# Optimization experiments

Hardware: AMD Instinct MI355X
Metric: run time of the kernel (lower is better)

Reference implementation:

```python
import jax, jax.numpy as jnp
import numpy as np

VOCAB = 256
PAD = 0
D_MODEL = 512
ATTN_DIM = 64
B, L = 8, 2048
LN_EPS = 1e-5


def layer_norm(x, g, b):
    mu = jnp.mean(x, axis=-1, keepdims=True)
    var = jnp.mean(jnp.square(x - mu), axis=-1, keepdims=True)
    return (x - mu) * jax.lax.rsqrt(var + LN_EPS) * g + b


def setup_inputs() -> dict:
    key = jax.random.key(0)
    ks = jax.random.split(key, 10)
    tokens = jax.random.randint(ks[0], (B, L), 1, VOCAB)  # avoid PAD=0
    prefix_lens = jax.random.randint(ks[1], (B,), 256, 1536)
    embed_w = jax.random.normal(ks[2], (VOCAB, D_MODEL), jnp.float32) * 0.02
    embed_w = embed_w.at[PAD].set(0.0)  # padding_idx row
    en_g = jnp.ones((D_MODEL,), jnp.float32)
    en_b = jnp.zeros((D_MODEL,), jnp.float32)
    fn_g = jnp.ones((D_MODEL,), jnp.float32)
    fn_b = jnp.zeros((D_MODEL,), jnp.float32)
    q_w = jax.random.normal(ks[3], (ATTN_DIM, D_MODEL), jnp.float32) * 0.02
    q_b = jnp.zeros((ATTN_DIM,), jnp.float32)
    k_w = jax.random.normal(ks[4], (ATTN_DIM, D_MODEL), jnp.float32) * 0.02
    k_b = jnp.zeros((ATTN_DIM,), jnp.float32)
    g_w = jax.random.normal(ks[5], (1, D_MODEL), jnp.float32) * 0.02
    g_b = jnp.full((1,), 2.0, jnp.float32)  # gate bias init to 2.0
    return dict(tokens=tokens, prefix_lens=prefix_lens, embed_w=embed_w,
                en_g=en_g, en_b=en_b, fn_g=fn_g, fn_b=fn_b,
                q_w=q_w, q_b=q_b, k_w=k_w, k_b=k_b, g_w=g_w, g_b=g_b)


def reference(tokens, prefix_lens, embed_w, en_g, en_b, fn_g, fn_b,
              q_w, q_b, k_w, k_b, g_w, g_b):
    # encode (n_layers=0: embed -> embed_norm -> final_norm)
    x = embed_w[tokens]                       # (B, L, D)
    x = layer_norm(x, en_g, en_b)
    h = layer_norm(x, fn_g, fn_b)

    vocab_logits = jnp.einsum('bld,vd->blv', h, embed_w)   # tied head
    q = h @ q_w.T + q_b                       # (B, L, A)
    k = h @ k_w.T + k_b                       # (B, L, A)
    scores = jnp.einsum('btd,bsd->bts', q, k) / np.sqrt(ATTN_DIM).astype(np.float32)

    idx = jnp.arange(L)[None, :]              # (1, L)
    prefix_mask = (idx < prefix_lens[:, None]) & (tokens != PAD)  # (B, L)
    scores = jnp.where(prefix_mask[:, None, :], scores, -jnp.inf)
    attn = jax.nn.softmax(scores, axis=-1)    # (B, L, L)

    prefix_onehot = jax.nn.one_hot(tokens, VOCAB, dtype=jnp.float32)
    prefix_onehot = prefix_onehot * prefix_mask[..., None]
    copy_dist = jnp.einsum('bts,bsv->btv', attn, prefix_onehot)  # (B, L, V)

    gate = jax.nn.sigmoid(h @ g_w.T + g_b)    # (B, L, 1)
    vocab_probs = jax.nn.softmax(vocab_logits, axis=-1)
    mixed = gate * vocab_probs + (1.0 - gate) * copy_dist
    mixed = jnp.clip(mixed, 1e-12, None)
    return jnp.log(mixed), gate[..., 0], attn
```

## Files before the change

### kernel.cpp

```cpp
#include <hip/hip_runtime.h>
#include <math.h>


#define DM 512
#define VC 256
#define SL 2048
#define NB 8
#define AD 64

typedef float f4v __attribute__((ext_vector_type(4)));

__device__ __forceinline__ float wave_sum(float v) {
#pragma unroll
  for (int o = 32; o > 0; o >>= 1) v += __shfl_xor(v, o, 64);
  return v;
}
__device__ __forceinline__ float wave_max(float v) {
#pragma unroll
  for (int o = 32; o > 0; o >>= 1) v = fmaxf(v, __shfl_xor(v, o, 64));
  return v;
}
__device__ __forceinline__ float blk_sum(float v, float* red) {
  v = wave_sum(v);
  if ((threadIdx.x & 63) == 0) red[threadIdx.x >> 6] = v;
  __syncthreads();
  float r = red[0] + red[1] + red[2] + red[3];
  __syncthreads();
  return r;
}
__device__ __forceinline__ float blk_max(float v, float* red) {
  v = wave_max(v);
  if ((threadIdx.x & 63) == 0) red[threadIdx.x >> 6] = v;
  __syncthreads();
  float r = fmaxf(fmaxf(red[0], red[1]), fmaxf(red[2], red[3]));
  __syncthreads();
  return r;
}

__global__ __launch_bounds__(256) void kprep(
    const float* __restrict__ embed_w, const float* __restrict__ q_w,
    const float* __restrict__ k_w, const int* __restrict__ tokens,
    const int* __restrict__ prefix_lens,
    float* __restrict__ embed_P, float* __restrict__ qk_P,
    int* __restrict__ cnt, int* __restrict__ ncnt,
    int* __restrict__ offs, int* __restrict__ list)
{
  __shared__ int c[VC];
  __shared__ int ca[VC];
  __shared__ int off[VC];
  __shared__ int cur[VC];
  const int blk = blockIdx.x;
  const int tid = threadIdx.x;
  if (blk < DM) {
    const int d = blk;
    embed_P[(((d >> 2) * VC + tid) << 2) + (d & 3)] = embed_w[tid * DM + d];
    if (tid < 128) {
      float val = (tid < 64) ? q_w[tid * DM + d] : k_w[(tid - 64) * DM + d];
      qk_P[(((d >> 2) * 128 + tid) << 2) + (d & 3)] = val;
    }
  } else {
    const int b = blk - DM;
    c[tid] = 0; ca[tid] = 0;
    __syncthreads();
    const int P = prefix_lens[b];
    const int4* trow = (const int4*)(tokens + b * SL);
#pragma unroll
    for (int i = tid; i < SL / 4; i += 256) {
      int4 tk = trow[i];
      int s0 = i * 4;
      atomicAdd(&ca[tk.x], 1); atomicAdd(&ca[tk.y], 1);
      atomicAdd(&ca[tk.z], 1); atomicAdd(&ca[tk.w], 1);
      if (s0     < P && tk.x != 0) atomicAdd(&c[tk.x], 1);
      if (s0 + 1 < P && tk.y != 0) atomicAdd(&c[tk.y], 1);
      if (s0 + 2 < P && tk.z != 0) atomicAdd(&c[tk.z], 1);
      if (s0 + 3 < P && tk.w != 0) atomicAdd(&c[tk.w], 1);
    }
    __syncthreads();
    int myc = ca[tid];
    off[tid] = myc;
    __syncthreads();
    for (int d2 = 1; d2 < VC; d2 <<= 1) {
      int add = (tid >= d2) ? off[tid - d2] : 0;
      __syncthreads();
      off[tid] += add;
      __syncthreads();
    }
    int excl = off[tid] - myc;
    cur[tid] = excl;
    __syncthreads();
#pragma unroll
    for (int i = tid; i < SL / 4; i += 256) {
      int4 tk = trow[i];
      int s0 = i * 4;
      int p;
      p = atomicAdd(&cur[tk.x], 1); list[b * SL + p] = s0;
      p = atomicAdd(&cur[tk.y], 1); list[b * SL + p] = s0 + 1;
      p = atomicAdd(&cur[tk.z], 1); list[b * SL + p] = s0 + 2;
      p = atomicAdd(&cur[tk.w], 1); list[b * SL + p] = s0 + 3;
    }
    __syncthreads();
    cnt [b * VC + tid] = c[tid];
    ncnt[b * VC + tid] = myc;
    offs[b * VC + tid] = excl;
  }
}

__global__ __launch_bounds__(256) void ktok(
    const float* __restrict__ embed_w,
    const float* __restrict__ en_g, const float* __restrict__ en_b,
    const float* __restrict__ fn_g, const float* __restrict__ fn_b,
    const float* __restrict__ q_b, const float* __restrict__ k_b,
    const float* __restrict__ g_w, const float* __restrict__ g_b,
    const float* __restrict__ embed_P, const float* __restrict__ qk_P,
    float* __restrict__ q_tok, float* __restrict__ kT_P,
    float* __restrict__ gate_tok, float* __restrict__ probs_tok)
{
  __shared__ float red[4];
  __shared__ __align__(16) float hs[DM];
  const int tt = blockIdx.x;
  const int tid = threadIdx.x;

  float x0 = embed_w[tt * DM + tid];
  float x1 = embed_w[tt * DM + 256 + tid];
  float mu = blk_sum(x0 + x1, red) * (1.0f / DM);
  float d0 = x0 - mu, d1 = x1 - mu;
  float var = blk_sum(d0 * d0 + d1 * d1, red) * (1.0f / DM);
  float inv = 1.0f / sqrtf(var + 1e-5f);
  float y0 = d0 * inv * en_g[tid] + en_b[tid];
  float y1 = d1 * inv * en_g[tid + 256] + en_b[tid + 256];
  mu = blk_sum(y0 + y1, red) * (1.0f / DM);
  d0 = y0 - mu; d1 = y1 - mu;
  var = blk_sum(d0 * d0 + d1 * d1, red) * (1.0f / DM);
  inv = 1.0f / sqrtf(var + 1e-5f);
  float h0 = d0 * inv * fn_g[tid] + fn_b[tid];
  float h1 = d1 * inv * fn_g[tid + 256] + fn_b[tid + 256];
  hs[tid] = h0; hs[tid + 256] = h1;
  float gp = blk_sum(h0 * g_w[tid] + h1 * g_w[tid + 256], red);
  if (tid == 0) gate_tok[tt] = 1.0f / (1.0f + expf(-(gp + g_b[0])));

  const float4* hs4 = (const float4*)hs;
  const float4* w4p = (const float4*)qk_P;
  const float4* e4p = (const float4*)embed_P;
  const bool qk_lane = (tid < 128);
  float acc = 0.0f;
  float lt = 0.0f;
#pragma unroll 8
  for (int d4 = 0; d4 < DM / 4; ++d4) {
    float4 h4 = hs4[d4];
    float4 e4 = e4p[d4 * VC + tid];
    lt += h4.x * e4.x + h4.y * e4.y + h4.z * e4.z + h4.w * e4.w;
    if (qk_lane) {
      float4 w4 = w4p[d4 * 128 + tid];
      acc += h4.x * w4.x + h4.y * w4.y + h4.z * w4.z + h4.w * w4.w;
    }
  }
  if (qk_lane) {
    if (tid < 64) {
      q_tok[tt * AD + tid] = acc + q_b[tid];
    } else {
      int a = tid - 64;
      kT_P[(((a >> 2) * VC + tt) << 2) + (a & 3)] = acc + k_b[a];
    }
  }
  float m = blk_max(lt, red);
  float e = expf(lt - m);
  float Z = blk_sum(e, red);
  probs_tok[tt * VC + tid] = e / Z;
}

__global__ __launch_bounds__(256) void kfused(
    const float* __restrict__ q_tok, const float* __restrict__ kT_P,
    const int* __restrict__ cnt, const int* __restrict__ ncnt,
    const int* __restrict__ offs, const int* __restrict__ list,
    const float* __restrict__ gate_tok, const float* __restrict__ probs_tok,
    const int* __restrict__ tokens, const int* __restrict__ prefix_lens,
    float* __restrict__ out_logmix, float* __restrict__ out_gate,
    float* __restrict__ out_attn)
{
  __shared__ float red[4];
  __shared__ __align__(16) float qs[AD];
  __shared__ __align__(16) float erow[VC];
  const int b = blockIdx.x >> 8, tt = blockIdx.x & 255;
  const int tid = threadIdx.x;

  const int P = prefix_lens[b];
  const int4* tokrow = (const int4*)(tokens + b * SL);
  int4 tk0 = tokrow[tid];
  int4 tk1 = tokrow[tid + 256];
  const int nr = ncnt[b * VC + tt];
  const int base_off = offs[b * VC + tt];
  const float pv = probs_tok[tt * VC + tid];
  const float g = gate_tok[tt];
  if (tid < AD) qs[tid] = q_tok[tt * AD + tid];
  __syncthreads();

  const float4* qs4 = (const float4*)qs;
  const float4* k4p = (const float4*)kT_P;
  float sv = 0.0f;
#pragma unroll
  for (int a4 = 0; a4 < AD / 4; ++a4) {
    float4 q4 = qs4[a4];
    float4 k4 = k4p[a4 * VC + tid];
    sv += q4.x * k4.x + q4.y * k4.y + q4.z * k4.z + q4.w * k4.w;
  }
  sv *= 0.125f;
  int c = cnt[b * VC + tid];
  float m = blk_max(c > 0 ? sv : -1e30f, red);
  float e = expf(sv - m);
  float Z = blk_sum((float)c * e, red);
  float en = e / Z;
  erow[tid] = en;
  float lv = logf(fmaxf(g * pv + (1.0f - g) * ((float)c * en), 1e-12f));
  __syncthreads();

  f4v a0, a1;
  {
    int s0 = tid * 4;
    a0.x = (s0     < P && tk0.x != 0) ? erow[tk0.x] : 0.0f;
    a0.y = (s0 + 1 < P && tk0.y != 0) ? erow[tk0.y] : 0.0f;
    a0.z = (s0 + 2 < P && tk0.z != 0) ? erow[tk0.z] : 0.0f;
    a0.w = (s0 + 3 < P && tk0.w != 0) ? erow[tk0.w] : 0.0f;
  }
  {
    int s0 = (tid + 256) * 4;
    a1.x = (s0     < P && tk1.x != 0) ? erow[tk1.x] : 0.0f;
    a1.y = (s0 + 1 < P && tk1.y != 0) ? erow[tk1.y] : 0.0f;
    a1.z = (s0 + 2 < P && tk1.z != 0) ? erow[tk1.z] : 0.0f;
    a1.w = (s0 + 3 < P && tk1.w != 0) ? erow[tk1.w] : 0.0f;
  }

  const int* lp = list + b * SL + base_off;
  for (int r = 0; r < nr; ++r) {
    int t = lp[r];
    size_t row = (size_t)(b * SL + t);
    __builtin_nontemporal_store(lv, &out_logmix[row * VC + tid]);
    if (tid == 0) out_gate[row] = g;
    f4v* ar = (f4v*)(out_attn + row * SL);
    __builtin_nontemporal_store(a0, &ar[tid]);
    __builtin_nontemporal_store(a1, &ar[tid + 256]);
  }
}

extern "C" void kernel_launch(void* const* d_in, const int* in_sizes, int n_in,
                              void* d_out, int out_size, void* d_ws, size_t ws_size,
                              hipStream_t stream)
{
  const int*   tokens      = (const int*)  d_in[0];
  const int*   prefix_lens = (const int*)  d_in[1];
  const float* embed_w     = (const float*)d_in[2];
  const float* en_g        = (const float*)d_in[3];
  const float* en_b        = (const float*)d_in[4];
  const float* fn_g        = (const float*)d_in[5];
  const float* fn_b        = (const float*)d_in[6];
  const float* q_b         = (const float*)d_in[8];
  const float* k_b         = (const float*)d_in[10];
  const float* q_w         = (const float*)d_in[7];
  const float* k_w         = (const float*)d_in[9];
  const float* g_w         = (const float*)d_in[11];
  const float* g_b         = (const float*)d_in[12];

  float* ws        = (float*)d_ws;
  float* embed_P   = ws;
  float* qk_P      = embed_P + DM * VC;
  float* kT_P      = qk_P + DM * 128;
  float* q_tok     = kT_P + AD * VC;
  float* gate_tok  = q_tok + VC * AD;
  float* probs_tok = gate_tok + VC;
  int*   cnt       = (int*)(probs_tok + VC * VC);
  int*   ncnt      = cnt + NB * VC;
  int*   offs      = ncnt + NB * VC;
  int*   list      = offs + NB * VC;

  float* out_logmix = (float*)d_out;
  float* out_gate   = out_logmix + (size_t)NB * SL * VC;
  float* out_attn   = out_gate + (size_t)NB * SL;

  kprep<<<DM + NB, 256, 0, stream>>>(embed_w, q_w, k_w, tokens, prefix_lens,
                                     embed_P, qk_P, cnt, ncnt, offs, list);
  ktok<<<VC, 256, 0, stream>>>(embed_w, en_g, en_b, fn_g, fn_b, q_b, k_b,
                               g_w, g_b, embed_P, qk_P,
                               q_tok, kT_P, gate_tok, probs_tok);
  kfused<<<NB * VC, 256, 0, stream>>>(q_tok, kT_P, cnt, ncnt, offs, list,
                                      gate_tok, probs_tok, tokens, prefix_lens,
                                      out_logmix, out_gate, out_attn);
}
```

Before: 238.5 us.

## Process four tokens per block in ktok and use single-wave blocks in kfused

ktok now handles four vocab tokens per 256-thread block, one wave each for the layer norms, and shares every embed_P/qk_P load across the four tokens. This cuts weight traffic and replaces block reductions with wave shuffles. kfused moves to 64-thread blocks where one wave computes all 256 scores and scatters wider rows, so its block-level syncs disappear. The trade is fewer resident threads per block and more registers per thread, while the output-write loop stays memory-bound.

```diff
diff --git a/kernel.cpp b/kernel.cpp
--- a/kernel.cpp
+++ b/kernel.cpp
@@ -20,20 +20,22 @@
   for (int o = 32; o > 0; o >>= 1) v = fmaxf(v, __shfl_xor(v, o, 64));
   return v;
 }
-__device__ __forceinline__ float blk_sum(float v, float* red) {
-  v = wave_sum(v);
-  if ((threadIdx.x & 63) == 0) red[threadIdx.x >> 6] = v;
-  __syncthreads();
-  float r = red[0] + red[1] + red[2] + red[3];
-  __syncthreads();
+__device__ __forceinline__ float hsum4(float4 a) {
+  return a.x + a.y + a.z + a.w;
+}
+__device__ __forceinline__ float4 subs4(float4 a, float s) {
+  float4 r; r.x = a.x - s; r.y = a.y - s; r.z = a.z - s; r.w = a.w - s;
   return r;
 }
-__device__ __forceinline__ float blk_max(float v, float* red) {
-  v = wave_max(v);
-  if ((threadIdx.x & 63) == 0) red[threadIdx.x >> 6] = v;
-  __syncthreads();
-  float r = fmaxf(fmaxf(red[0], red[1]), fmaxf(red[2], red[3]));
-  __syncthreads();
+__device__ __forceinline__ float dot44(float4 a, float4 b) {
+  return a.x * b.x + a.y * b.y + a.z * b.z + a.w * b.w;
+}
+__device__ __forceinline__ float4 lnmap4(float4 d, float inv, float4 g, float4 b) {
+  float4 r;
+  r.x = d.x * inv * g.x + b.x;
+  r.y = d.y * inv * g.y + b.y;
+  r.z = d.z * inv * g.z + b.z;
+  r.w = d.w * inv * g.w + b.w;
   return r;
 }
 
@@ -115,60 +117,90 @@
     float* __restrict__ q_tok, float* __restrict__ kT_P,
     float* __restrict__ gate_tok, float* __restrict__ probs_tok)
 {
-  __shared__ float red[4];
-  __shared__ __align__(16) float hs[DM];
-  const int tt = blockIdx.x;
+  __shared__ __align__(16) float hs[4 * DM];
+  __shared__ __align__(16) float lts[4 * VC];
+  const int t0 = blockIdx.x * 4;
   const int tid = threadIdx.x;
-
-  float x0 = embed_w[tt * DM + tid];
-  float x1 = embed_w[tt * DM + 256 + tid];
-  float mu = blk_sum(x0 + x1, red) * (1.0f / DM);
-  float d0 = x0 - mu, d1 = x1 - mu;
-  float var = blk_sum(d0 * d0 + d1 * d1, red) * (1.0f / DM);
+  const int w = tid >> 6;
+  const int l = tid & 63;
+  const int tt = t0 + w;
+
+  const float4* ew4 = (const float4*)(embed_w + (size_t)tt * DM);
+  float4 x0 = ew4[l];
+  float4 x1 = ew4[l + 64];
+  float mu = wave_sum(hsum4(x0) + hsum4(x1)) * (1.0f / DM);
+  float4 d0 = subs4(x0, mu), d1 = subs4(x1, mu);
+  float var = wave_sum(dot44(d0, d0) + dot44(d1, d1)) * (1.0f / DM);
   float inv = 1.0f / sqrtf(var + 1e-5f);
-  float y0 = d0 * inv * en_g[tid] + en_b[tid];
-  float y1 = d1 * inv * en_g[tid + 256] + en_b[tid + 256];
-  mu = blk_sum(y0 + y1, red) * (1.0f / DM);
-  d0 = y0 - mu; d1 = y1 - mu;
-  var = blk_sum(d0 * d0 + d1 * d1, red) * (1.0f / DM);
+  float4 y0 = lnmap4(d0, inv, ((const float4*)en_g)[l],      ((const float4*)en_b)[l]);
+  float4 y1 = lnmap4(d1, inv, ((const float4*)en_g)[l + 64], ((const float4*)en_b)[l + 64]);
+  mu = wave_sum(hsum4(y0) + hsum4(y1)) * (1.0f / DM);
+  d0 = subs4(y0, mu); d1 = subs4(y1, mu);
+  var = wave_sum(dot44(d0, d0) + dot44(d1, d1)) * (1.0f / DM);
   inv = 1.0f / sqrtf(var + 1e-5f);
-  float h0 = d0 * inv * fn_g[tid] + fn_b[tid];
-  float h1 = d1 * inv * fn_g[tid + 256] + fn_b[tid + 256];
-  hs[tid] = h0; hs[tid + 256] = h1;
-  float gp = blk_sum(h0 * g_w[tid] + h1 * g_w[tid + 256], red);
-  if (tid == 0) gate_tok[tt] = 1.0f / (1.0f + expf(-(gp + g_b[0])));
+  float4 h0 = lnmap4(d0, inv, ((const float4*)fn_g)[l],      ((const float4*)fn_b)[l]);
+  float4 h1 = lnmap4(d1, inv, ((const float4*)fn_g)[l + 64], ((const float4*)fn_b)[l + 64]);
+  float gp = wave_sum(dot44(h0, ((const float4*)g_w)[l]) +
+                      dot44(h1, ((const float4*)g_w)[l + 64]));
+  if (l == 0) gate_tok[tt] = 1.0f / (1.0f + expf(-(gp + g_b[0])));
+  ((float4*)hs)[w * 128 + l]      = h0;
+  ((float4*)hs)[w * 128 + 64 + l] = h1;
+  __syncthreads();
 
   const float4* hs4 = (const float4*)hs;
+  const float4* e4p = (const float4*)embed_P;
   const float4* w4p = (const float4*)qk_P;
-  const float4* e4p = (const float4*)embed_P;
   const bool qk_lane = (tid < 128);
-  float acc = 0.0f;
-  float lt = 0.0f;
-#pragma unroll 8
+  float lt[4] = {0.f, 0.f, 0.f, 0.f};
+  float aq[4] = {0.f, 0.f, 0.f, 0.f};
+#pragma unroll 4
   for (int d4 = 0; d4 < DM / 4; ++d4) {
-    float4 h4 = hs4[d4];
     float4 e4 = e4p[d4 * VC + tid];
-    lt += h4.x * e4.x + h4.y * e4.y + h4.z * e4.z + h4.w * e4.w;
+    float4 hA = hs4[d4];
+    float4 hB = hs4[128 + d4];
+    float4 hC = hs4[256 + d4];
+    float4 hD = hs4[384 + d4];
+    lt[0] += dot44(hA, e4);
+    lt[1] += dot44(hB, e4);
+    lt[2] += dot44(hC, e4);
+    lt[3] += dot44(hD, e4);
     if (qk_lane) {
       float4 w4 = w4p[d4 * 128 + tid];
-      acc += h4.x * w4.x + h4.y * w4.y + h4.z * w4.z + h4.w * w4.w;
-    }
-  }
-  if (qk_lane) {
-    if (tid < 64) {
-      q_tok[tt * AD + tid] = acc + q_b[tid];
-    } else {
-      int a = tid - 64;
-      kT_P[(((a >> 2) * VC + tt) << 2) + (a & 3)] = acc + k_b[a];
-    }
-  }
-  float m = blk_max(lt, red);
-  float e = expf(lt - m);
-  float Z = blk_sum(e, red);
-  probs_tok[tt * VC + tid] = e / Z;
-}
-
-__global__ __launch_bounds__(256) void kfused(
+      aq[0] += dot44(hA, w4);
+      aq[1] += dot44(hB, w4);
+      aq[2] += dot44(hC, w4);
+      aq[3] += dot44(hD, w4);
+    }
+  }
+  if (tid < 64) {
+    float qb = q_b[tid];
+#pragma unroll
+    for (int t = 0; t < 4; ++t) q_tok[(t0 + t) * AD + tid] = aq[t] + qb;
+  } else if (tid < 128) {
+    int a = tid - 64;
+    float kb = k_b[a];
+#pragma unroll
+    for (int t = 0; t < 4; ++t)
+      kT_P[(((a >> 2) * VC + (t0 + t)) << 2) + (a & 3)] = aq[t] + kb;
+  }
+#pragma unroll
+  for (int t = 0; t < 4; ++t) lts[t * VC + tid] = lt[t];
+  __syncthreads();
+
+  float p0 = lts[w * VC + l];
+  float p1 = lts[w * VC + 64 + l];
+  float p2 = lts[w * VC + 128 + l];
+  float p3 = lts[w * VC + 192 + l];
+  float m = wave_max(fmaxf(fmaxf(p0, p1), fmaxf(p2, p3)));
+  float e0 = expf(p0 - m), e1 = expf(p1 - m), e2 = expf(p2 - m), e3 = expf(p3 - m);
+  float Z = wave_sum(e0 + e1 + e2 + e3);
+  probs_tok[tt * VC + l]       = e0 / Z;
+  probs_tok[tt * VC + 64 + l]  = e1 / Z;
+  probs_tok[tt * VC + 128 + l] = e2 / Z;
+  probs_tok[tt * VC + 192 + l] = e3 / Z;
+}
+
+__global__ __launch_bounds__(64) void kfused(
     const float* __restrict__ q_tok, const float* __restrict__ kT_P,
     const int* __restrict__ cnt, const int* __restrict__ ncnt,
     const int* __restrict__ offs, const int* __restrict__ list,
@@ -177,67 +209,85 @@
     float* __restrict__ out_logmix, float* __restrict__ out_gate,
     float* __restrict__ out_attn)
 {
-  __shared__ float red[4];
   __shared__ __align__(16) float qs[AD];
   __shared__ __align__(16) float erow[VC];
+  __shared__ __align__(16) float lvs[VC];
   const int b = blockIdx.x >> 8, tt = blockIdx.x & 255;
-  const int tid = threadIdx.x;
+  const int l = threadIdx.x;
 
   const int P = prefix_lens[b];
   const int4* tokrow = (const int4*)(tokens + b * SL);
-  int4 tk0 = tokrow[tid];
-  int4 tk1 = tokrow[tid + 256];
+  int4 tk[8];
+#pragma unroll
+  for (int i = 0; i < 8; ++i) tk[i] = tokrow[l + (i << 6)];
   const int nr = ncnt[b * VC + tt];
   const int base_off = offs[b * VC + tt];
-  const float pv = probs_tok[tt * VC + tid];
   const float g = gate_tok[tt];
-  if (tid < AD) qs[tid] = q_tok[tt * AD + tid];
+  int   c_[4];
+  float pv[4];
+#pragma unroll
+  for (int j = 0; j < 4; ++j) {
+    c_[j] = cnt[b * VC + l + (j << 6)];
+    pv[j] = probs_tok[tt * VC + l + (j << 6)];
+  }
+  qs[l] = q_tok[tt * AD + l];
   __syncthreads();
 
   const float4* qs4 = (const float4*)qs;
   const float4* k4p = (const float4*)kT_P;
-  float sv = 0.0f;
+  float sv[4] = {0.f, 0.f, 0.f, 0.f};
 #pragma unroll
   for (int a4 = 0; a4 < AD / 4; ++a4) {
     float4 q4 = qs4[a4];
-    float4 k4 = k4p[a4 * VC + tid];
-    sv += q4.x * k4.x + q4.y * k4.y + q4.z * k4.z + q4.w * k4.w;
-  }
-  sv *= 0.125f;
-  int c = cnt[b * VC + tid];
-  float m = blk_max(c > 0 ? sv : -1e30f, red);
-  float e = expf(sv - m);
-  float Z = blk_sum((float)c * e, red);
-  float en = e / Z;
-  erow[tid] = en;
-  float lv = logf(fmaxf(g * pv + (1.0f - g) * ((float)c * en), 1e-12f));
+    sv[0] += dot44(q4, k4p[a4 * VC + l]);
+    sv[1] += dot44(q4, k4p[a4 * VC + 64 + l]);
+    sv[2] += dot44(q4, k4p[a4 * VC + 128 + l]);
+    sv[3] += dot44(q4, k4p[a4 * VC + 192 + l]);
+  }
+  float mloc = -1e30f;
+#pragma unroll
+  for (int j = 0; j < 4; ++j) {
+    sv[j] *= 0.125f;
+    mloc = fmaxf(mloc, c_[j] > 0 ? sv[j] : -1e30f);
+  }
+  float m = wave_max(mloc);
+  float e[4], zloc = 0.f;
+#pragma unroll
+  for (int j = 0; j < 4; ++j) {
+    e[j] = expf(sv[j] - m);
+    zloc += (float)c_[j] * e[j];
+  }
+  float Z = wave_sum(zloc);
+#pragma unroll
+  for (int j = 0; j < 4; ++j) {
+    float en = e[j] / Z;
+    erow[l + (j << 6)] = en;
+    lvs[l + (j << 6)] =
+        logf(fmaxf(g * pv[j] + (1.0f - g) * ((float)c_[j] * en), 1e-12f));
+  }
   __syncthreads();
 
-  f4v a0, a1;
-  {
-    int s0 = tid * 4;
-    a0.x = (s0     < P && tk0.x != 0) ? erow[tk0.x] : 0.0f;
-    a0.y = (s0 + 1 < P && tk0.y != 0) ? erow[tk0.y] : 0.0f;
-    a0.z = (s0 + 2 < P && tk0.z != 0) ? erow[tk0.z] : 0.0f;
-    a0.w = (s0 + 3 < P && tk0.w != 0) ? erow[tk0.w] : 0.0f;
-  }
-  {
-    int s0 = (tid + 256) * 4;
-    a1.x = (s0     < P && tk1.x != 0) ? erow[tk1.x] : 0.0f;
-    a1.y = (s0 + 1 < P && tk1.y != 0) ? erow[tk1.y] : 0.0f;
-    a1.z = (s0 + 2 < P && tk1.z != 0) ? erow[tk1.z] : 0.0f;
-    a1.w = (s0 + 3 < P && tk1.w != 0) ? erow[tk1.w] : 0.0f;
+  f4v lv4 = ((const f4v*)lvs)[l];
+  f4v a[8];
+#pragma unroll
+  for (int i = 0; i < 8; ++i) {
+    int s0 = (l + (i << 6)) << 2;
+    a[i].x = (s0     < P && tk[i].x != 0) ? erow[tk[i].x] : 0.0f;
+    a[i].y = (s0 + 1 < P && tk[i].y != 0) ? erow[tk[i].y] : 0.0f;
+    a[i].z = (s0 + 2 < P && tk[i].z != 0) ? erow[tk[i].z] : 0.0f;
+    a[i].w = (s0 + 3 < P && tk[i].w != 0) ? erow[tk[i].w] : 0.0f;
   }
 
   const int* lp = list + b * SL + base_off;
   for (int r = 0; r < nr; ++r) {
     int t = lp[r];
     size_t row = (size_t)(b * SL + t);
-    __builtin_nontemporal_store(lv, &out_logmix[row * VC + tid]);
-    if (tid == 0) out_gate[row] = g;
+    __builtin_nontemporal_store(lv4, &((f4v*)(out_logmix + row * VC))[l]);
+    if (l == 0) out_gate[row] = g;
     f4v* ar = (f4v*)(out_attn + row * SL);
-    __builtin_nontemporal_store(a0, &ar[tid]);
-    __builtin_nontemporal_store(a1, &ar[tid + 256]);
+#pragma unroll
+    for (int i = 0; i < 8; ++i)
+      __builtin_nontemporal_store(a[i], &ar[l + (i << 6)]);
   }
 }
 
@@ -277,10 +327,10 @@
 
   kprep<<<DM + NB, 256, 0, stream>>>(embed_w, q_w, k_w, tokens, prefix_lens,
                                      embed_P, qk_P, cnt, ncnt, offs, list);
-  ktok<<<VC, 256, 0, stream>>>(embed_w, en_g, en_b, fn_g, fn_b, q_b, k_b,
-                               g_w, g_b, embed_P, qk_P,
-                               q_tok, kT_P, gate_tok, probs_tok);
-  kfused<<<NB * VC, 256, 0, stream>>>(q_tok, kT_P, cnt, ncnt, offs, list,
-                                      gate_tok, probs_tok, tokens, prefix_lens,
-                                      out_logmix, out_gate, out_attn);
-}
+  ktok<<<VC / 4, 256, 0, stream>>>(embed_w, en_g, en_b, fn_g, fn_b, q_b, k_b,
+                                   g_w, g_b, embed_P, qk_P,
+                                   q_tok, kT_P, gate_tok, probs_tok);
+  kfused<<<NB * VC, 64, 0, stream>>>(q_tok, kT_P, cnt, ncnt, offs, list,
+                                     gate_tok, probs_tok, tokens, prefix_lens,
+                                     out_logmix, out_gate, out_attn);
+}
```

Result: slower. 250.9 us (+5.2%).
